# Optimization experiments

Hardware: AMD Instinct MI355X
Metric: run time of the kernel (lower is better)

## Reference

```python
import jax, jax.numpy as jnp
import numpy as np

N_NODES = 50000
N_EDGES = 600000
EMB_DIM = 128
HIDDEN = 128
BN_EPS = 1e-5


def setup_inputs() -> dict:
    key = jax.random.key(0)
    ks = jax.random.split(key, 8)
    s_in = 1.0 / np.sqrt(EMB_DIM)
    s_h = 1.0 / np.sqrt(HIDDEN)
    return {
        "x_idx": jnp.arange(N_NODES, dtype=jnp.int32),
        "edge_index": jax.random.randint(ks[0], (2, N_EDGES), 0, N_NODES, dtype=jnp.int32),
        "emb_table": jax.random.normal(ks[1], (N_NODES, EMB_DIM), jnp.float32),
        # ClusterGCNConv: lin_out (bias=False) and lin_root (bias=False)
        "W_out": jax.random.uniform(ks[2], (HIDDEN, EMB_DIM), jnp.float32, -s_in, s_in),
        "W_root": jax.random.uniform(ks[3], (HIDDEN, EMB_DIM), jnp.float32, -s_in, s_in),
        "bn0_gamma": jnp.ones((HIDDEN,), jnp.float32),
        "bn0_beta": jnp.zeros((HIDDEN,), jnp.float32),
        # SGConv 1 (K=1, add_self_loops=True, Linear with bias)
        "W_sg1": jax.random.uniform(ks[4], (HIDDEN, HIDDEN), jnp.float32, -s_h, s_h),
        "b_sg1": jnp.zeros((HIDDEN,), jnp.float32),
        "bn1_gamma": jnp.ones((HIDDEN,), jnp.float32),
        "bn1_beta": jnp.zeros((HIDDEN,), jnp.float32),
        # SGConv 2 (final layer)
        "W_sg2": jax.random.uniform(ks[5], (HIDDEN, HIDDEN), jnp.float32, -s_h, s_h),
        "b_sg2": jnp.zeros((HIDDEN,), jnp.float32),
    }


def _cluster_gcn(x, row, col, W_out, W_root, n):
    # PyG ClusterGCNConv (add_self_loops=False, diag_lambda=0, bias=False):
    # out[c] = sum_{(r->c)} (1/deg(c)) * x[r];  return out @ W_out^T + x @ W_root^T
    deg = jax.ops.segment_sum(jnp.ones_like(col, dtype=x.dtype), col, num_segments=n)
    deg_inv = 1.0 / jnp.maximum(deg, 1.0)
    msg = x[row] * deg_inv[col][:, None]                  # [E, D]
    agg = jax.ops.segment_sum(msg, col, num_segments=n)   # [N, D]
    return agg @ W_out.T + x @ W_root.T


def _sg_conv(x, row, col, W, b, n):
    # PyG SGConv K=1 with gcn_norm: A_hat = D^{-1/2}(A+I)D^{-1/2}, then Linear.
    loop = jnp.arange(n, dtype=row.dtype)
    r = jnp.concatenate([row, loop])
    c = jnp.concatenate([col, loop])
    deg = jax.ops.segment_sum(jnp.ones_like(c, dtype=x.dtype), c, num_segments=n)
    dis = jnp.where(deg > 0, jax.lax.rsqrt(jnp.maximum(deg, 1e-12)), 0.0)
    ew = dis[r] * dis[c]                                   # [E+N]
    agg = jax.ops.segment_sum(x[r] * ew[:, None], c, num_segments=n)
    return agg @ W.T + b


def _bn(x, gamma, beta):
    # BatchNorm1d in training mode: batch statistics, biased variance.
    mu = x.mean(axis=0)
    var = ((x - mu) ** 2).mean(axis=0)
    return (x - mu) * jax.lax.rsqrt(var + BN_EPS) * gamma + beta


def reference(x_idx, edge_index, emb_table, W_out, W_root, bn0_gamma, bn0_beta,
              W_sg1, b_sg1, bn1_gamma, bn1_beta, W_sg2, b_sg2):
    n = emb_table.shape[0]
    row, col = edge_index[0], edge_index[1]
    x = emb_table[x_idx]                                   # [N, D]
    # layer 0: ClusterGCNConv -> BN -> ReLU (dropout p=0)
    x = _cluster_gcn(x, row, col, W_out, W_root, n)
    x = jax.nn.relu(_bn(x, bn0_gamma, bn0_beta))
    # layer 1: SGConv -> BN -> ReLU
    x = _sg_conv(x, row, col, W_sg1, b_sg1, n)
    x = jax.nn.relu(_bn(x, bn1_gamma, bn1_beta))
    # final SGConv
    return _sg_conv(x, row, col, W_sg2, b_sg2, n)
```

## Files before the change

kernel.cpp:

```cpp
#include <hip/hip_runtime.h>
#include <stdint.h>

#define NN 50000
#define NE 600000
#define DD 128
#define BN_EPS 1e-5f

typedef __attribute__((ext_vector_type(8))) short short8;
typedef __attribute__((ext_vector_type(4))) float f32x4;

__device__ __forceinline__ float bf2f(uint16_t u) {
    union { uint32_t u; float f; } v; v.u = ((uint32_t)u) << 16; return v.f;
}
__device__ __forceinline__ uint16_t f2bf(float f) {
    union { float f; uint32_t u; } v; v.f = f;
    return (uint16_t)((v.u + 0x7FFFu + ((v.u >> 16) & 1u)) >> 16);
}
__device__ __forceinline__ float lo16(uint32_t v) { return bf2f((uint16_t)(v & 0xFFFFu)); }
__device__ __forceinline__ float hi16(uint32_t v) { return bf2f((uint16_t)(v >> 16)); }

__global__ void k_zero(uint4* __restrict__ p, int n16) {
    int i = blockIdx.x * 256 + threadIdx.x;
    if (i < n16) p[i] = make_uint4(0u, 0u, 0u, 0u);
}

#define EB ((NE + 255) / 256)
#define VB ((NN * 32) / 256)
#define WB 32
__global__ void k_pre(const int* __restrict__ ei, int* __restrict__ cnt,
                      const int* __restrict__ x_idx, const float* __restrict__ emb,
                      uint16_t* __restrict__ xb,
                      const float* __restrict__ Wa, const float* __restrict__ Wb_,
                      const float* __restrict__ Wc, const float* __restrict__ Wd,
                      uint16_t* __restrict__ wb) {
    int b = blockIdx.x;
    if (b < EB) {
        int e = b * 256 + threadIdx.x;
        if (e < NE) atomicAdd(&cnt[ei[NE + e]], 1);
    } else if (b < EB + VB) {
        int idx = (b - EB) * 256 + threadIdx.x;
        int node = idx >> 5, c4 = (idx & 31) << 2;
        int src = x_idx[node];
        float4 v = *(const float4*)(emb + (size_t)src * DD + c4);
        ushort4 o;
        o.x = f2bf(v.x); o.y = f2bf(v.y); o.z = f2bf(v.z); o.w = f2bf(v.w);
        *(ushort4*)(xb + (size_t)node * DD + c4) = o;
    } else {
        int idx = (b - EB - VB) * 256 + threadIdx.x;
        int w = idx >> 11, rem = idx & 2047;
        const float* src = (w == 0) ? Wa : (w == 1) ? Wb_ : (w == 2) ? Wc : Wd;
        float4 v0 = *(const float4*)(src + rem * 8);
        float4 v1 = *(const float4*)(src + rem * 8 + 4);
        uint4 pk;
        pk.x = (uint32_t)f2bf(v0.x) | ((uint32_t)f2bf(v0.y) << 16);
        pk.y = (uint32_t)f2bf(v0.z) | ((uint32_t)f2bf(v0.w) << 16);
        pk.z = (uint32_t)f2bf(v1.x) | ((uint32_t)f2bf(v1.y) << 16);
        pk.w = (uint32_t)f2bf(v1.z) | ((uint32_t)f2bf(v1.w) << 16);
        int row = rem >> 4, c16 = rem & 15;
        uint32_t boff = (uint32_t)(row * 256 + ((c16 * 16) ^ ((row & 7) << 4)));
        *(uint4*)((char*)wb + (size_t)w * 32768 + boff) = pk;
    }
}

__global__ void k_alloc(const int* __restrict__ cnt, int* __restrict__ cursor,
                        int* __restrict__ off, int* __restrict__ fillp,
                        float* __restrict__ deginv, float* __restrict__ dis) {
    int i = blockIdx.x * 256 + threadIdx.x;
    int lane = threadIdx.x & 63;
    int deg = (i < NN) ? cnt[i] : 0;
    int v = deg;
    #pragma unroll
    for (int d = 1; d < 64; d <<= 1) {
        int t = __shfl_up(v, d, 64);
        if (lane >= d) v += t;
    }
    int total = __shfl(v, 63, 64);
    int wbase = 0;
    if (lane == 63) wbase = atomicAdd(cursor, total);
    wbase = __shfl(wbase, 63, 64);
    int base = wbase + v - deg;
    if (i < NN) {
        off[i] = base;
        fillp[i] = base;
        deginv[i] = 1.0f / fmaxf((float)deg, 1.0f);
        dis[i] = rsqrtf((float)deg + 1.0f);
    }
}

__global__ void k_fill(const int* __restrict__ ei, int* __restrict__ fillp,
                       int* __restrict__ csr_row) {
    int e = blockIdx.x * 256 + threadIdx.x;
    if (e < NE) {
        int c = ei[NE + e];
        int p = atomicAdd(&fillp[c], 1);
        csr_row[p] = ei[e];
    }
}

template<int MODE>
__global__ __launch_bounds__(256)
void k_agg(const uint16_t* __restrict__ X, const int* __restrict__ off,
           const int* __restrict__ cnt, const int* __restrict__ csr_row,
           const float* __restrict__ deginv, const float* __restrict__ dis,
           uint16_t* __restrict__ aggb) {
    int gw = blockIdx.x * 4 + (threadIdx.x >> 6);
    int lane = threadIdx.x & 63;
    int ql = lane & 15;
    int node = gw * 4 + (lane >> 4);
    if (node >= NN) return;
    float a0 = 0.0f, a1 = 0.0f, a2 = 0.0f, a3 = 0.0f;
    float a4 = 0.0f, a5 = 0.0f, a6 = 0.0f, a7 = 0.0f;
    if (MODE == 1) {
        uint4 v = ((const uint4*)(X + (size_t)node * DD))[ql];
        a0 = lo16(v.x); a1 = hi16(v.x); a2 = lo16(v.y); a3 = hi16(v.y);
        a4 = lo16(v.z); a5 = hi16(v.z); a6 = lo16(v.w); a7 = hi16(v.w);
    }
    int s = off[node], deg = cnt[node];
    int m = max(deg, __shfl(deg, lane ^ 16, 64));
    m = max(m, __shfl(m, lane ^ 32, 64));
    for (int b = 0; b < m; b += 16) {
        int c16 = min(deg - b, 16);
        int idxv = (ql < c16) ? csr_row[s + b + ql] : 0;
        int steps = min(m - b, 16);
        int i = 0;
        for (; i + 8 <= steps; i += 8) {
            uint4 v[8]; float w[8];
            #pragma unroll
            for (int u = 0; u < 8; ++u) {
                int r = __shfl(idxv, (lane & 48) + i + u, 64);
                w[u] = (b + i + u < deg) ? 1.0f : 0.0f;
                v[u] = ((const uint4*)(X + (size_t)r * DD))[ql];
            }
            #pragma unroll
            for (int u = 0; u < 8; ++u) {
                a0 = fmaf(w[u], lo16(v[u].x), a0); a1 = fmaf(w[u], hi16(v[u].x), a1);
                a2 = fmaf(w[u], lo16(v[u].y), a2); a3 = fmaf(w[u], hi16(v[u].y), a3);
                a4 = fmaf(w[u], lo16(v[u].z), a4); a5 = fmaf(w[u], hi16(v[u].z), a5);
                a6 = fmaf(w[u], lo16(v[u].w), a6); a7 = fmaf(w[u], hi16(v[u].w), a7);
            }
        }
        if (i + 4 <= steps) {
            uint4 v[4]; float w[4];
            #pragma unroll
            for (int u = 0; u < 4; ++u) {
                int r = __shfl(idxv, (lane & 48) + i + u, 64);
                w[u] = (b + i + u < deg) ? 1.0f : 0.0f;
                v[u] = ((const uint4*)(X + (size_t)r * DD))[ql];
            }
            #pragma unroll
            for (int u = 0; u < 4; ++u) {
                a0 = fmaf(w[u], lo16(v[u].x), a0); a1 = fmaf(w[u], hi16(v[u].x), a1);
                a2 = fmaf(w[u], lo16(v[u].y), a2); a3 = fmaf(w[u], hi16(v[u].y), a3);
                a4 = fmaf(w[u], lo16(v[u].z), a4); a5 = fmaf(w[u], hi16(v[u].z), a5);
                a6 = fmaf(w[u], lo16(v[u].w), a6); a7 = fmaf(w[u], hi16(v[u].w), a7);
            }
            i += 4;
        }
        for (; i < steps; ++i) {
            int r = __shfl(idxv, (lane & 48) + i, 64);
            float w = (b + i < deg) ? 1.0f : 0.0f;
            uint4 v = ((const uint4*)(X + (size_t)r * DD))[ql];
            a0 = fmaf(w, lo16(v.x), a0); a1 = fmaf(w, hi16(v.x), a1);
            a2 = fmaf(w, lo16(v.y), a2); a3 = fmaf(w, hi16(v.y), a3);
            a4 = fmaf(w, lo16(v.z), a4); a5 = fmaf(w, hi16(v.z), a5);
            a6 = fmaf(w, lo16(v.w), a6); a7 = fmaf(w, hi16(v.w), a7);
        }
    }
    float sc = (MODE == 1) ? dis[node] : deginv[node];
    a0 *= sc; a1 *= sc; a2 *= sc; a3 *= sc;
    a4 *= sc; a5 *= sc; a6 *= sc; a7 *= sc;
    uint4 o;
    o.x = (uint32_t)f2bf(a0) | ((uint32_t)f2bf(a1) << 16);
    o.y = (uint32_t)f2bf(a2) | ((uint32_t)f2bf(a3) << 16);
    o.z = (uint32_t)f2bf(a4) | ((uint32_t)f2bf(a5) << 16);
    o.w = (uint32_t)f2bf(a6) | ((uint32_t)f2bf(a7) << 16);
    ((uint4*)(aggb + (size_t)node * DD))[ql] = o;
}

template<bool DUAL, bool STATS, bool BIAS, bool STORE_BF16>
__global__ __launch_bounds__(256, DUAL ? 2 : 3)
void k_gemm(const uint16_t* __restrict__ A1, const uint16_t* __restrict__ A2,
            const uint16_t* __restrict__ Wb1, const uint16_t* __restrict__ Wb2,
            const float* __restrict__ bias, float* __restrict__ Hf,
            uint16_t* __restrict__ Hb, float* __restrict__ stats) {
    constexpr int NW = DUAL ? 2 : 1;
    __shared__ uint16_t Wlds[NW * 128 * 128];
    const int t = threadIdx.x;
    const int lane = t & 63, wid = t >> 6;
    const int l15 = lane & 15, kgrp = lane >> 4;
    const int wm = (wid >> 1) * 64, wn = (wid & 1) * 64;
    const int m0 = blockIdx.x * 128;

    #pragma unroll
    for (int w = 0; w < NW; ++w) {
        const char* Ws = (const char*)(w ? Wb2 : Wb1);
        char* ldsb = (char*)Wlds + w * 32768;
        #pragma unroll
        for (int it = 0; it < 8; ++it) {
            int base_chunk = it * 256 + (t & 192);
            int lane_chunk = base_chunk + (t & 63);
            __builtin_amdgcn_global_load_lds(
                (const __attribute__((address_space(1))) uint32_t*)(Ws + (size_t)lane_chunk * 16),
                (__attribute__((address_space(3))) uint32_t*)(uint32_t)(uintptr_t)(ldsb + base_chunk * 16),
                16, 0, 0);
        }
    }
    short8 a1r[4][4];
    #pragma unroll
    for (int m = 0; m < 4; ++m) {
        int row = min(m0 + wm + m * 16 + l15, NN - 1);
        const uint16_t* ap = A1 + (size_t)row * DD + kgrp * 8;
        #pragma unroll
        for (int ks = 0; ks < 4; ++ks)
            a1r[m][ks] = *(const short8*)(ap + ks * 32);
    }
    __syncthreads();

    f32x4 acc[4][4];
    #pragma unroll
    for (int m = 0; m < 4; ++m)
        #pragma unroll
        for (int n = 0; n < 4; ++n) acc[m][n] = f32x4{0.0f, 0.0f, 0.0f, 0.0f};

    short8 a2r[4][4];
    if (DUAL) {
        #pragma unroll
        for (int m = 0; m < 4; ++m) {
            int row = min(m0 + wm + m * 16 + l15, NN - 1);
            const uint16_t* ap = A2 + (size_t)row * DD + kgrp * 8;
            #pragma unroll
            for (int ks = 0; ks < 4; ++ks)
                a2r[m][ks] = *(const short8*)(ap + ks * 32);
        }
    }
    #pragma unroll
    for (int ph = 0; ph < NW; ++ph) {
        #pragma unroll
        for (int ks = 0; ks < 4; ++ks) {
            short8 b[4];
            int kb = ks * 64 + (kgrp << 4);
            #pragma unroll
            for (int n = 0; n < 4; ++n) {
                int row = wn + n * 16 + l15;
                b[n] = *(const short8*)((const char*)Wlds + ph * 32768
                                        + row * 256 + (kb ^ ((row & 7) << 4)));
            }
            #pragma unroll
            for (int m = 0; m < 4; ++m)
                #pragma unroll
                for (int n = 0; n < 4; ++n)
                    acc[m][n] = __builtin_amdgcn_mfma_f32_16x16x32_bf16(
                        (ph ? a2r : a1r)[m][ks], b[n], acc[m][n], 0, 0, 0);
        }
    }
    float* stc = STATS ? stats + ((wid + ((blockIdx.x & 1) << 2)) & 7) * 256 : nullptr;
    #pragma unroll
    for (int n = 0; n < 4; ++n) {
        int col = wn + n * 16 + l15;
        float bb = BIAS ? bias[col] : 0.0f;
        float ssum = 0.0f, ssq = 0.0f;
        #pragma unroll
        for (int m = 0; m < 4; ++m) {
            int rbase = m0 + wm + m * 16 + kgrp * 4;
            #pragma unroll
            for (int i = 0; i < 4; ++i) {
                int gr = rbase + i;
                if (gr < NN) {
                    float v = acc[m][n][i] + bb;
                    if (STORE_BF16) Hb[(size_t)gr * DD + col] = f2bf(v);
                    else            Hf[(size_t)gr * DD + col] = v;
                    ssum += v; ssq += v * v;
                }
            }
        }
        if (STATS) {
            ssum += __shfl_xor(ssum, 16, 64);
            ssum += __shfl_xor(ssum, 32, 64);
            ssq  += __shfl_xor(ssq, 16, 64);
            ssq  += __shfl_xor(ssq, 32, 64);
            if (lane < 16) {
                atomicAdd(&stc[col], ssum);
                atomicAdd(&stc[128 + col], ssq);
            }
        }
    }
}

__global__ __launch_bounds__(256)
void k_bnrelu(const uint16_t* __restrict__ Hb, const float* __restrict__ st,
              const float* __restrict__ gamma, const float* __restrict__ beta,
              const float* __restrict__ dis, uint16_t* __restrict__ xb) {
    __shared__ float s_sc[128], s_of[128];
    int t = threadIdx.x;
    if (t < 128) {
        const float invn = 1.0f / (float)NN;
        float sum = 0.0f, sq = 0.0f;
        #pragma unroll
        for (int k = 0; k < 8; ++k) {
            sum += st[k * 256 + t];
            sq  += st[k * 256 + 128 + t];
        }
        float mean = sum * invn;
        float var = sq * invn - mean * mean;
        float sc = gamma[t] * rsqrtf(var + BN_EPS);
        s_sc[t] = sc;
        s_of[t] = beta[t] - mean * sc;
    }
    __syncthreads();
    int idx = blockIdx.x * 256 + t;
    int node = idx >> 4, c8 = (idx & 15) << 3;
    if (node >= NN) return;
    float d = dis[node];
    uint4 h = *(const uint4*)(Hb + (size_t)node * DD + c8);
    uint32_t hw[4] = {h.x, h.y, h.z, h.w};
    uint32_t ow[4];
    #pragma unroll
    for (int j = 0; j < 4; ++j) {
        int c = c8 + j * 2;
        float v0 = fmaxf(lo16(hw[j]) * s_sc[c]     + s_of[c],     0.0f) * d;
        float v1 = fmaxf(hi16(hw[j]) * s_sc[c + 1] + s_of[c + 1], 0.0f) * d;
        ow[j] = (uint32_t)f2bf(v0) | ((uint32_t)f2bf(v1) << 16);
    }
    uint4 o = make_uint4(ow[0], ow[1], ow[2], ow[3]);
    *(uint4*)(xb + (size_t)node * DD + c8) = o;
}

extern "C" void kernel_launch(void* const* d_in, const int* in_sizes, int n_in,
                              void* d_out, int out_size, void* d_ws, size_t ws_size,
                              hipStream_t stream) {
    const int* x_idx   = (const int*)d_in[0];
    const int* ei      = (const int*)d_in[1];
    const float* emb   = (const float*)d_in[2];
    const float* W_out = (const float*)d_in[3];
    const float* W_root= (const float*)d_in[4];
    const float* g0    = (const float*)d_in[5];
    const float* be0   = (const float*)d_in[6];
    const float* W1    = (const float*)d_in[7];
    const float* b1    = (const float*)d_in[8];
    const float* g1    = (const float*)d_in[9];
    const float* be1   = (const float*)d_in[10];
    const float* W2    = (const float*)d_in[11];
    const float* b2    = (const float*)d_in[12];
    float* out = (float*)d_out;

    char* ws = (char*)d_ws;
    size_t o = 0;
    auto carve = [&](size_t bytes) -> void* {
        void* p = ws + o;
        o = (o + bytes + 255) & ~(size_t)255;
        return p;
    };
    int* cnt      = (int*)carve((size_t)NN * 4);
    int* cursor   = (int*)carve(4);
    float* st0    = (float*)carve(2048 * 4);
    float* st1    = (float*)carve(2048 * 4);
    size_t zlen = o;
    int* fillp    = (int*)carve((size_t)NN * 4);
    int* off      = (int*)carve((size_t)NN * 4);
    float* deginv = (float*)carve((size_t)NN * 4);
    float* dis    = (float*)carve((size_t)NN * 4);
    int* csr_row  = (int*)carve((size_t)NE * 4);
    uint16_t* xb  = (uint16_t*)carve((size_t)NN * DD * 2);
    uint16_t* aggb= (uint16_t*)carve((size_t)NN * DD * 2);
    uint16_t* hb  = (uint16_t*)carve((size_t)NN * DD * 2);
    uint16_t* wb  = (uint16_t*)carve((size_t)4 * 16384 * 2);

    const int ZB = (int)((zlen / 16 + 255) / 256);
    const int NB = (NN + 255) / 256;
    const int GB = (NN + 127) / 128;
    const int AB = (NN + 15) / 16;
    const int BB = (NN * 16 + 255) / 256;

    k_zero<<<ZB, 256, 0, stream>>>((uint4*)ws, (int)(zlen / 16));
    k_pre<<<EB + VB + WB, 256, 0, stream>>>(ei, cnt, x_idx, emb, xb,
                                            W_out, W_root, W1, W2, wb);
    k_alloc<<<NB, 256, 0, stream>>>(cnt, cursor, off, fillp, deginv, dis);
    k_fill<<<EB, 256, 0, stream>>>(ei, fillp, csr_row);

    k_agg<0><<<AB, 256, 0, stream>>>(xb, off, cnt, csr_row, deginv, dis, aggb);
    k_gemm<true, true, false, true><<<GB, 256, 0, stream>>>(
        aggb, xb, wb, wb + 16384, nullptr, nullptr, hb, st0);
    k_bnrelu<<<BB, 256, 0, stream>>>(hb, st0, g0, be0, dis, xb);

    k_agg<1><<<AB, 256, 0, stream>>>(xb, off, cnt, csr_row, deginv, dis, aggb);
    k_gemm<false, true, true, true><<<GB, 256, 0, stream>>>(
        aggb, nullptr, wb + 32768, nullptr, b1, nullptr, hb, st1);
    k_bnrelu<<<BB, 256, 0, stream>>>(hb, st1, g1, be1, dis, xb);

    k_agg<1><<<AB, 256, 0, stream>>>(xb, off, cnt, csr_row, deginv, dis, aggb);
    k_gemm<false, false, true, false><<<GB, 256, 0, stream>>>(
        aggb, nullptr, wb + 49152, nullptr, b2, out, nullptr, nullptr);
}
```

Measured before the change: 225.1 us.

## Sort nodes by degree so aggregation wavefronts get balanced work

Builds a degree histogram, prefix-scans it in a single block, and computes a permutation that groups nodes by in-degree (capped at 511). Each aggregation wavefront handles four nodes and loops to the largest degree among them, so grouping similar degrees is meant to cut the idle lanes caused by that mismatch. In exchange it adds a small scan kernel, extra atomics on the histogram, and an indirect perm lookup per node. It also scatters which nodes a wavefront handles, which lowers locality of the per-node output writes.

```diff
diff --git a/kernel.cpp b/kernel.cpp
--- a/kernel.cpp
+++ b/kernel.cpp
@@ -27,6 +27,7 @@
 #define EB ((NE + 255) / 256)
 #define VB ((NN * 32) / 256)
 #define WB 32
+#define NB ((NN + 255) / 256)
 __global__ void k_pre(const int* __restrict__ ei, int* __restrict__ cnt,
                       const int* __restrict__ x_idx, const float* __restrict__ emb,
                       uint16_t* __restrict__ xb,
@@ -64,7 +65,8 @@
 
 __global__ void k_alloc(const int* __restrict__ cnt, int* __restrict__ cursor,
                         int* __restrict__ off, int* __restrict__ fillp,
-                        float* __restrict__ deginv, float* __restrict__ dis) {
+                        float* __restrict__ deginv, float* __restrict__ dis,
+                        int* __restrict__ hist) {
     int i = blockIdx.x * 256 + threadIdx.x;
     int lane = threadIdx.x & 63;
     int deg = (i < NN) ? cnt[i] : 0;
@@ -84,16 +86,43 @@
         fillp[i] = base;
         deginv[i] = 1.0f / fmaxf((float)deg, 1.0f);
         dis[i] = rsqrtf((float)deg + 1.0f);
-    }
+        atomicAdd(&hist[min(deg, 511)], 1);
+    }
+}
+
+__global__ void k_hscan(int* __restrict__ hist) {
+    __shared__ int s[512];
+    int t = threadIdx.x;
+    int v = hist[t];
+    s[t] = v;
+    __syncthreads();
+    for (int d = 1; d < 512; d <<= 1) {
+        int add = (t >= d) ? s[t - d] : 0;
+        __syncthreads();
+        s[t] += add;
+        __syncthreads();
+    }
+    hist[t] = s[t] - v;
 }
 
 __global__ void k_fill(const int* __restrict__ ei, int* __restrict__ fillp,
-                       int* __restrict__ csr_row) {
-    int e = blockIdx.x * 256 + threadIdx.x;
-    if (e < NE) {
-        int c = ei[NE + e];
-        int p = atomicAdd(&fillp[c], 1);
-        csr_row[p] = ei[e];
+                       int* __restrict__ csr_row, const int* __restrict__ cnt,
+                       int* __restrict__ hist, int* __restrict__ perm) {
+    int b = blockIdx.x;
+    if (b < EB) {
+        int e = b * 256 + threadIdx.x;
+        if (e < NE) {
+            int c = ei[NE + e];
+            int p = atomicAdd(&fillp[c], 1);
+            csr_row[p] = ei[e];
+        }
+    } else {
+        int i = (b - EB) * 256 + threadIdx.x;
+        if (i < NN) {
+            int dg = min(cnt[i], 511);
+            int sidx = atomicAdd(&hist[dg], 1);
+            perm[sidx] = i;
+        }
     }
 }
 
@@ -101,13 +130,15 @@
 __global__ __launch_bounds__(256)
 void k_agg(const uint16_t* __restrict__ X, const int* __restrict__ off,
            const int* __restrict__ cnt, const int* __restrict__ csr_row,
+           const int* __restrict__ perm,
            const float* __restrict__ deginv, const float* __restrict__ dis,
            uint16_t* __restrict__ aggb) {
     int gw = blockIdx.x * 4 + (threadIdx.x >> 6);
     int lane = threadIdx.x & 63;
     int ql = lane & 15;
-    int node = gw * 4 + (lane >> 4);
-    if (node >= NN) return;
+    int slot = gw * 4 + (lane >> 4);
+    if (slot >= NN) return;
+    int node = perm[slot];
     float a0 = 0.0f, a1 = 0.0f, a2 = 0.0f, a3 = 0.0f;
     float a4 = 0.0f, a5 = 0.0f, a6 = 0.0f, a7 = 0.0f;
     if (MODE == 1) {
@@ -354,19 +385,20 @@
     int* cursor   = (int*)carve(4);
     float* st0    = (float*)carve(2048 * 4);
     float* st1    = (float*)carve(2048 * 4);
+    int* hist     = (int*)carve(512 * 4);
     size_t zlen = o;
     int* fillp    = (int*)carve((size_t)NN * 4);
     int* off      = (int*)carve((size_t)NN * 4);
     float* deginv = (float*)carve((size_t)NN * 4);
     float* dis    = (float*)carve((size_t)NN * 4);
     int* csr_row  = (int*)carve((size_t)NE * 4);
+    int* perm     = (int*)carve((size_t)NN * 4);
     uint16_t* xb  = (uint16_t*)carve((size_t)NN * DD * 2);
     uint16_t* aggb= (uint16_t*)carve((size_t)NN * DD * 2);
     uint16_t* hb  = (uint16_t*)carve((size_t)NN * DD * 2);
     uint16_t* wb  = (uint16_t*)carve((size_t)4 * 16384 * 2);
 
     const int ZB = (int)((zlen / 16 + 255) / 256);
-    const int NB = (NN + 255) / 256;
     const int GB = (NN + 127) / 128;
     const int AB = (NN + 15) / 16;
     const int BB = (NN * 16 + 255) / 256;
@@ -374,20 +406,21 @@
     k_zero<<<ZB, 256, 0, stream>>>((uint4*)ws, (int)(zlen / 16));
     k_pre<<<EB + VB + WB, 256, 0, stream>>>(ei, cnt, x_idx, emb, xb,
                                             W_out, W_root, W1, W2, wb);
-    k_alloc<<<NB, 256, 0, stream>>>(cnt, cursor, off, fillp, deginv, dis);
-    k_fill<<<EB, 256, 0, stream>>>(ei, fillp, csr_row);
-
-    k_agg<0><<<AB, 256, 0, stream>>>(xb, off, cnt, csr_row, deginv, dis, aggb);
+    k_alloc<<<NB, 256, 0, stream>>>(cnt, cursor, off, fillp, deginv, dis, hist);
+    k_hscan<<<1, 512, 0, stream>>>(hist);
+    k_fill<<<EB + NB, 256, 0, stream>>>(ei, fillp, csr_row, cnt, hist, perm);
+
+    k_agg<0><<<AB, 256, 0, stream>>>(xb, off, cnt, csr_row, perm, deginv, dis, aggb);
     k_gemm<true, true, false, true><<<GB, 256, 0, stream>>>(
         aggb, xb, wb, wb + 16384, nullptr, nullptr, hb, st0);
     k_bnrelu<<<BB, 256, 0, stream>>>(hb, st0, g0, be0, dis, xb);
 
-    k_agg<1><<<AB, 256, 0, stream>>>(xb, off, cnt, csr_row, deginv, dis, aggb);
+    k_agg<1><<<AB, 256, 0, stream>>>(xb, off, cnt, csr_row, perm, deginv, dis, aggb);
     k_gemm<false, true, true, true><<<GB, 256, 0, stream>>>(
         aggb, nullptr, wb + 32768, nullptr, b1, nullptr, hb, st1);
     k_bnrelu<<<BB, 256, 0, stream>>>(hb, st1, g1, be1, dis, xb);
 
-    k_agg<1><<<AB, 256, 0, stream>>>(xb, off, cnt, csr_row, deginv, dis, aggb);
+    k_agg<1><<<AB, 256, 0, stream>>>(xb, off, cnt, csr_row, perm, deginv, dis, aggb);
     k_gemm<false, false, true, false><<<GB, 256, 0, stream>>>(
         aggb, nullptr, wb + 49152, nullptr, b2, out, nullptr, nullptr);
 }
```

Measured after the change: 528.1 us. 135% more time.
